# Performance work log

Measured on AMD Instinct MI355X. Metric: run time of the kernel, lower is better.

The kernel has to match this reference:

```python
import jax, jax.numpy as jnp
import numpy as np

N, D, E, TOP_K = 16384, 1024, 8, 2

def setup_inputs() -> dict:
    key = jax.random.key(0)
    ks = jax.random.split(key, 8)
    sc = 1.0 / np.sqrt(D)
    return {
        "x": jax.random.normal(ks[0], (N, D), dtype=jnp.float32),
        "context_vector": jax.random.uniform(ks[1], (E,), dtype=jnp.float32),
        "router_w": jax.random.uniform(ks[2], (E, D), minval=-sc, maxval=sc),
        "router_b": jax.random.uniform(ks[3], (E,), minval=-sc, maxval=sc),
        "expert_w": jax.random.uniform(ks[4], (E, D, D), minval=-sc, maxval=sc),
        "expert_b": jax.random.uniform(ks[5], (E, D), minval=-sc, maxval=sc),
        "context_weight": jax.random.uniform(ks[6], (1,), dtype=jnp.float32),
    }

def reference(x, context_vector, router_w, router_b, expert_w, expert_b, context_weight):
    # Router: gate logits with conceptual context bias. [N, E]
    gate_logits = x @ router_w.T + router_b + context_weight * context_vector
    weights = jax.nn.softmax(gate_logits, axis=-1)

    # Top-k selection and renormalization. [N, k]
    top_k_weights, top_k_indices = jax.lax.top_k(weights, TOP_K)
    top_k_weights = top_k_weights / jnp.sum(top_k_weights, axis=-1, keepdims=True)

    # All-expert outputs (dense grouped GEMM): y[n,e,:] = x[n] @ W[e].T + b[e]
    all_out = jnp.einsum('nd,efd->nef', x, expert_w) + expert_b  # [N, E, D]

    # Gather the top-k expert outputs per token and combine. [N, k, D]
    gathered = jnp.take_along_axis(all_out, top_k_indices[:, :, None], axis=1)
    expert_outputs = jnp.sum(top_k_weights[:, :, None] * gathered, axis=1)  # [N, D]

    # Load-balancing loss: avg router prob . fraction of tokens routed per expert
    avg_router_prob = weights.mean(axis=0)  # [E]
    assignment_mask = jax.nn.one_hot(top_k_indices, E).sum(axis=1)  # [N, E]
    fraction_routed = assignment_mask.mean(axis=0)  # [E]
    load_loss = jnp.sum(avg_router_prob * fraction_routed)

    return expert_outputs, load_loss
```

## Files before the change

### kernel.cpp

```cpp
#include <hip/hip_runtime.h>
#include <stdint.h>

#define N_TOK 16384
#define DDIM  1024
#define NEXP  8
#define CNT_STRIDE 64

#define BM 128
#define BN 128
#define BK 64
#define MAX_TILES 264
#define EP_PITCH 72

typedef __bf16 bf16x8 __attribute__((ext_vector_type(8)));
typedef float  f32x4  __attribute__((ext_vector_type(4)));

__device__ __forceinline__ unsigned short f2bf(float f) {
  union { float f; uint32_t u; } a; a.f = f;
  uint32_t u = a.u;
  u += 0x7fffu + ((u >> 16) & 1u);
  return (unsigned short)(u >> 16);
}

__device__ __forceinline__ float bf2f(unsigned short u) {
  union { uint32_t u; float f; } a; a.u = ((uint32_t)u) << 16;
  return a.f;
}

__device__ __forceinline__ float2 bfpair(uint32_t u) {
  union { uint32_t u; float f; } lo, hi;
  lo.u = u << 16; hi.u = u & 0xffff0000u;
  return make_float2(lo.f, hi.f);
}

__device__ __forceinline__ void load_lds16(const void* g, void* l) {
  __builtin_amdgcn_global_load_lds(
      (const __attribute__((address_space(1))) void*)g,
      (__attribute__((address_space(3))) void*)l,
      16, 0, 0);
}

__global__ __launch_bounds__(512) void router_kernel(
    const float* __restrict__ x, const float* __restrict__ rw,
    const float* __restrict__ rb, const float* __restrict__ cv,
    const float* __restrict__ cwp,
    const float4* __restrict__ ew4, ushort4* __restrict__ wb4,
    unsigned short* __restrict__ xg,
    int* __restrict__ perm_idx, float* __restrict__ perm_w,
    int* __restrict__ inv_idx,
    int* __restrict__ cnt, float* __restrict__ sum_w)
{
  __shared__ int   sCnt[NEXP];
  __shared__ int   sBase[NEXP];
  __shared__ float sSW[NEXP];
  __shared__ int   sE0[32], sE1[32], sR0[32], sR1[32];
  __shared__ float sW0[32], sW1[32];

  const int tid = threadIdx.x;
  if (tid < NEXP) { sCnt[tid] = 0; sSW[tid] = 0.0f; }
  __syncthreads();

  const int wave = tid >> 6;
  const int lane = tid & 63;

  float lsw[NEXP];
#pragma unroll
  for (int e = 0; e < NEXP; ++e) lsw[e] = 0.0f;

  const float cw = cwp[0];

  for (int t = 0; t < 4; ++t) {
    const int i = wave * 4 + t;
    const int n = blockIdx.x * 32 + i;

    float p[NEXP];
#pragma unroll
    for (int e = 0; e < NEXP; ++e) p[e] = 0.0f;

    const float2* x2 = (const float2*)(x + (size_t)n * DDIM);
    uint32_t* xgp = (uint32_t*)(xg + (size_t)n * DDIM);

    float2 xv[8];
#pragma unroll
    for (int it = 0; it < 8; ++it) xv[it] = x2[lane + 64 * it];
#pragma unroll
    for (int it = 0; it < 8; ++it) {
      int dp = lane + 64 * it;
      xgp[dp] = (uint32_t)f2bf(xv[it].x) | ((uint32_t)f2bf(xv[it].y) << 16);
#pragma unroll
      for (int e = 0; e < NEXP; ++e) {
        float2 wv = ((const float2*)(rw + e * DDIM))[dp];
        p[e] = fmaf(xv[it].x, wv.x, fmaf(xv[it].y, wv.y, p[e]));
      }
    }
#pragma unroll
    for (int e = 0; e < NEXP; ++e) {
#pragma unroll
      for (int off = 32; off > 0; off >>= 1)
        p[e] += __shfl_xor(p[e], off, 64);
    }

    if (lane == 0) {
      float w[NEXP];
      float m = -1e30f;
#pragma unroll
      for (int e = 0; e < NEXP; ++e) {
        w[e] = p[e] + rb[e] + cw * cv[e];
        m = fmaxf(m, w[e]);
      }
      float s = 0.0f;
#pragma unroll
      for (int e = 0; e < NEXP; ++e) { w[e] = expf(w[e] - m); s += w[e]; }
      float inv = 1.0f / s;
#pragma unroll
      for (int e = 0; e < NEXP; ++e) { w[e] *= inv; lsw[e] += w[e]; }
      int e0 = 0;
#pragma unroll
      for (int e = 1; e < NEXP; ++e) if (w[e] > w[e0]) e0 = e;
      int e1 = (e0 == 0) ? 1 : 0;
#pragma unroll
      for (int e = 0; e < NEXP; ++e) if (e != e0 && w[e] > w[e1]) e1 = e;
      float rsum = 1.0f / (w[e0] + w[e1]);
      int r0 = atomicAdd(&sCnt[e0], 1);
      int r1 = atomicAdd(&sCnt[e1], 1);
      sE0[i] = e0; sE1[i] = e1; sR0[i] = r0; sR1[i] = r1;
      sW0[i] = w[e0] * rsum; sW1[i] = w[e1] * rsum;
    }
  }

  if (lane == 0) {
#pragma unroll
    for (int e = 0; e < NEXP; ++e) atomicAdd(&sSW[e], lsw[e]);
  }
  __syncthreads();

  if (tid < NEXP) {
    sBase[tid] = atomicAdd(&cnt[tid * CNT_STRIDE], sCnt[tid]);
    atomicAdd(&sum_w[tid * CNT_STRIDE], sSW[tid]);
  }
  __syncthreads();

  if (tid < 64) {
    int i = tid >> 1, k = tid & 1;
    int e = k ? sE1[i] : sE0[i];
    int r = k ? sR1[i] : sR0[i];
    float wv = k ? sW1[i] : sW0[i];
    int pos = sBase[e] + r;
    int n = blockIdx.x * 32 + i;
    perm_idx[e * N_TOK + pos] = n;
    perm_w [e * N_TOK + pos] = wv;
    inv_idx[2 * n + k] = (e << 14) | pos;
  }

  size_t base = (size_t)blockIdx.x * 512 + tid;
#pragma unroll
  for (int i2 = 0; i2 < 8; ++i2) {
    size_t idx = base + (size_t)i2 * 262144;
    float4 v = ew4[idx];
    wb4[idx] = make_ushort4(f2bf(v.x), f2bf(v.y), f2bf(v.z), f2bf(v.w));
  }
}

template<int MODE>
__global__ __launch_bounds__(256) void moe_gemm_kernel(
    const unsigned short* __restrict__ xg, const unsigned short* __restrict__ wb,
    const float* __restrict__ eb,
    const int* __restrict__ perm_idx, const float* __restrict__ perm_w,
    const int* __restrict__ cnt,
    unsigned short* __restrict__ ybuf, float* __restrict__ out)
{
  const int id = blockIdx.x;
  const int tn = id / MAX_TILES;
  const int tileIdx = id - tn * MAX_TILES;

  int e = -1, tm = 0, count = 0, ebase = 0, pref = 0;
#pragma unroll
  for (int j = 0; j < NEXP; ++j) {
    int c = cnt[j * CNT_STRIDE];
    int t = (c + BM - 1) >> 7;
    if (e < 0 && tileIdx < pref + t) { e = j; tm = tileIdx - pref; count = c; }
    if (e < 0) ebase += c;
    pref += t;
  }
  if (e < 0) return;

  __shared__ union {
    struct { __bf16 As[BM * BK]; __bf16 Bs[BN * BK]; } g;
    __bf16 ep[4 * 64 * EP_PITCH];
  } sm;
  __shared__ int   tokS[BM];
  __shared__ float wtS[BM];

  const int tid = threadIdx.x;
  const int wave = tid >> 6;
  const int lane = tid & 63;

  if (tid < BM) {
    int row = tm * BM + tid;
    int rc = row < count ? row : count - 1;
    tokS[tid] = perm_idx[e * N_TOK + rc];
    wtS[tid] = (row < count) ? perm_w[e * N_TOK + row] : 0.0f;
  }
  __syncthreads();

  const unsigned short* aptr[4];
  const unsigned short* bptr[4];
  const unsigned short* wbase = wb + (size_t)e * DDIM * DDIM;
#pragma unroll
  for (int t = 0; t < 4; ++t) {
    int r = wave * 32 + t * 8 + (lane >> 3);
    int cg = (lane & 7) ^ (r & 7);
    aptr[t] = xg + (size_t)tokS[r] * DDIM + cg * 8;
    bptr[t] = wbase + (size_t)(tn * BN + r) * DDIM + cg * 8;
  }

  const int mw = (wave >> 1) * 64;
  const int nw = (wave & 1) * 64;
  const int quad = lane >> 4;
  const int l15 = lane & 15;

  f32x4 acc[4][4] = {};

  for (int kk = 0; kk < DDIM; kk += BK) {
#pragma unroll
    for (int t = 0; t < 4; ++t) {
      load_lds16(aptr[t], &sm.g.As[(wave * 32 + t * 8) * BK]);
      load_lds16(bptr[t], &sm.g.Bs[(wave * 32 + t * 8) * BK]);
      aptr[t] += BK; bptr[t] += BK;
    }
    __syncthreads();

#pragma unroll
    for (int ks = 0; ks < 2; ++ks) {
      bf16x8 af[4], bfr[4];
#pragma unroll
      for (int mi = 0; mi < 4; ++mi) {
        int m = mw + mi * 16 + l15;
        int slot = (ks * 4 + quad) ^ (m & 7);
        af[mi] = *(const bf16x8*)&sm.g.As[m * BK + slot * 8];
      }
#pragma unroll
      for (int ni = 0; ni < 4; ++ni) {
        int n = nw + ni * 16 + l15;
        int slot = (ks * 4 + quad) ^ (n & 7);
        bfr[ni] = *(const bf16x8*)&sm.g.Bs[n * BK + slot * 8];
      }
#pragma unroll
      for (int mi = 0; mi < 4; ++mi)
#pragma unroll
        for (int ni = 0; ni < 4; ++ni)
          acc[mi][ni] = __builtin_amdgcn_mfma_f32_16x16x32_bf16(bfr[ni], af[mi], acc[mi][ni], 0, 0, 0);
    }
    __syncthreads();
  }

  const int valid = count - tm * BM;

  if (MODE == 1) {
    __bf16* slab = &sm.ep[wave * (64 * EP_PITCH)];
#pragma unroll
    for (int mi = 0; mi < 4; ++mi) {
      float wt = wtS[mw + mi * 16 + l15];
#pragma unroll
      for (int ni = 0; ni < 4; ++ni) {
        int gcol = tn * BN + nw + ni * 16 + quad * 4;
        const float4 bv = *(const float4*)&eb[e * DDIM + gcol];
        ushort4 pk;
        pk.x = f2bf((acc[mi][ni][0] + bv.x) * wt);
        pk.y = f2bf((acc[mi][ni][1] + bv.y) * wt);
        pk.z = f2bf((acc[mi][ni][2] + bv.z) * wt);
        pk.w = f2bf((acc[mi][ni][3] + bv.w) * wt);
        *(ushort4*)&slab[(mi * 16 + l15) * EP_PITCH + ni * 16 + quad * 4] = pk;
      }
    }
    const int gb = ebase + tm * BM;
#pragma unroll
    for (int s = 0; s < 8; ++s) {
      int lrow = s * 8 + (lane >> 3);
      uint4 v = *(const uint4*)&slab[lrow * EP_PITCH + (lane & 7) * 8];
      int brow = mw + lrow;
      if (brow < valid)
        *(uint4*)&ybuf[(size_t)(gb + brow) * DDIM + tn * BN + nw + (lane & 7) * 8] = v;
    }
  } else {
#pragma unroll
    for (int mi = 0; mi < 4; ++mi) {
      int brow = mw + mi * 16 + l15;
      float wt = wtS[brow];
      int tok = tokS[brow];
#pragma unroll
      for (int ni = 0; ni < 4; ++ni) {
        int gcol = tn * BN + nw + ni * 16 + quad * 4;
        const float4 bv = *(const float4*)&eb[e * DDIM + gcol];
        if (brow < valid) {
          atomicAdd(out + (size_t)tok * DDIM + gcol + 0, (acc[mi][ni][0] + bv.x) * wt);
          atomicAdd(out + (size_t)tok * DDIM + gcol + 1, (acc[mi][ni][1] + bv.y) * wt);
          atomicAdd(out + (size_t)tok * DDIM + gcol + 2, (acc[mi][ni][2] + bv.z) * wt);
          atomicAdd(out + (size_t)tok * DDIM + gcol + 3, (acc[mi][ni][3] + bv.w) * wt);
        }
      }
    }
  }
}

__global__ __launch_bounds__(256) void combine_kernel(
    const unsigned short* __restrict__ ybuf, const int* __restrict__ inv_idx,
    const int* __restrict__ cnt, float* __restrict__ out)
{
  const int wave = threadIdx.x >> 6;
  const int lane = threadIdx.x & 63;
  const int n = blockIdx.x * 4 + wave;

  int base[NEXP];
  int acc = 0;
#pragma unroll
  for (int j = 0; j < NEXP; ++j) { base[j] = acc; acc += cnt[j * CNT_STRIDE]; }

  int i0 = inv_idx[2 * n];
  int i1 = inv_idx[2 * n + 1];
  int g0 = base[i0 >> 14] + (i0 & 16383);
  int g1 = base[i1 >> 14] + (i1 & 16383);

  const uint4* r0 = (const uint4*)(ybuf + (size_t)g0 * DDIM);
  const uint4* r1 = (const uint4*)(ybuf + (size_t)g1 * DDIM);
  float4* o = (float4*)(out + (size_t)n * DDIM);

#pragma unroll
  for (int it = 0; it < 2; ++it) {
    int c = lane + 64 * it;
    uint4 a = r0[c];
    uint4 b = r1[c];
    float2 a0 = bfpair(a.x), a1 = bfpair(a.y), a2 = bfpair(a.z), a3 = bfpair(a.w);
    float2 b0 = bfpair(b.x), b1 = bfpair(b.y), b2 = bfpair(b.z), b3 = bfpair(b.w);
    float4 v0, v1;
    v0.x = a0.x + b0.x; v0.y = a0.y + b0.y; v0.z = a1.x + b1.x; v0.w = a1.y + b1.y;
    v1.x = a2.x + b2.x; v1.y = a2.y + b2.y; v1.z = a3.x + b3.x; v1.w = a3.y + b3.y;
    o[2 * c] = v0;
    o[2 * c + 1] = v1;
  }
}

__global__ void loss_kernel(const float* __restrict__ sum_w,
                            const int* __restrict__ cnt,
                            float* __restrict__ out) {
  if (threadIdx.x == 0 && blockIdx.x == 0) {
    float l = 0.0f;
#pragma unroll
    for (int e = 0; e < NEXP; ++e)
      l += sum_w[e * CNT_STRIDE] * (float)cnt[e * CNT_STRIDE];
    out[(size_t)N_TOK * DDIM] = l * (1.0f / ((float)N_TOK * (float)N_TOK));
  }
}

extern "C" void kernel_launch(void* const* d_in, const int* in_sizes, int n_in,
                              void* d_out, int out_size, void* d_ws, size_t ws_size,
                              hipStream_t stream) {
  const float* x  = (const float*)d_in[0];
  const float* cv = (const float*)d_in[1];
  const float* rw = (const float*)d_in[2];
  const float* rb = (const float*)d_in[3];
  const float* ew = (const float*)d_in[4];
  const float* eb = (const float*)d_in[5];
  const float* cw = (const float*)d_in[6];
  float* out = (float*)d_out;

  char* ws = (char*)d_ws;
  unsigned short* xg = (unsigned short*)ws;
  unsigned short* wb = (unsigned short*)(ws + 33554432);
  int*   perm_idx = (int*)  (ws + 50331648);
  float* perm_w   = (float*)(ws + 50855936);
  int*   inv_idx  = (int*)  (ws + 51380224);
  int*   cnt      = (int*)  (ws + 51511296);
  float* sum_w    = (float*)(ws + 51513344);
  unsigned short* ybuf = (unsigned short*)(ws + 51515392);
  const size_t NEED = 51515392ull + 67108864ull;

  const bool big = ws_size >= NEED;

  hipMemsetAsync(cnt, 0, 4096, stream);
  if (!big)
    hipMemsetAsync(d_out, 0, (size_t)N_TOK * DDIM * sizeof(float), stream);

  router_kernel<<<N_TOK / 32, 512, 0, stream>>>(x, rw, rb, cv, cw,
                                                (const float4*)ew, (ushort4*)wb,
                                                xg, perm_idx, perm_w, inv_idx, cnt, sum_w);

  if (big) {
    moe_gemm_kernel<1><<<MAX_TILES * 8, 256, 0, stream>>>(
        xg, wb, eb, perm_idx, perm_w, cnt, ybuf, out);
    combine_kernel<<<N_TOK / 4, 256, 0, stream>>>(ybuf, inv_idx, cnt, out);
  } else {
    moe_gemm_kernel<0><<<MAX_TILES * 8, 256, 0, stream>>>(
        xg, wb, eb, perm_idx, perm_w, cnt, ybuf, out);
  }

  loss_kernel<<<1, 64, 0, stream>>>(sum_w, cnt, out);
}
```

Before: 288.7 us.

## Use 256x256 tiles with double-buffered LDS and interleaved MFMA/load pipeline

Enlarges the grouped-GEMM tile from 128x128 to 256x256 with 512 threads and double-buffers the A/B LDS tiles. The K loop is split into four phases, each issuing a slice of the next tile's global-to-LDS loads between MFMA groups, with hand-placed s_waitcnt barriers and raised wave priority around the MFMA blocks. This is meant to raise arithmetic intensity and hide global load latency behind compute. In exchange it uses more LDS and registers per block, pads partially filled expert tiles more heavily at the larger tile size, and produces fewer blocks, which can hurt load balance across CUs.

```diff
diff --git a/kernel.cpp b/kernel.cpp
--- a/kernel.cpp
+++ b/kernel.cpp
@@ -6,10 +6,11 @@
 #define NEXP  8
 #define CNT_STRIDE 64
 
-#define BM 128
-#define BN 128
+#define BM 256
+#define BN 256
 #define BK 64
-#define MAX_TILES 264
+#define NKT 16
+#define MAX_TILES 136
 #define EP_PITCH 72
 
 typedef __bf16 bf16x8 __attribute__((ext_vector_type(8)));
@@ -39,6 +40,11 @@
       (__attribute__((address_space(3))) void*)l,
       16, 0, 0);
 }
+
+#define SCHED_FENCE() __builtin_amdgcn_sched_barrier(0)
+#define BAR_PLAIN() do { SCHED_FENCE(); asm volatile("s_barrier" ::: "memory"); SCHED_FENCE(); } while (0)
+#define BAR_LGKM0() do { SCHED_FENCE(); asm volatile("s_waitcnt lgkmcnt(0)\n\ts_barrier" ::: "memory"); SCHED_FENCE(); } while (0)
+#define BAR_VM(N)   do { SCHED_FENCE(); asm volatile("s_waitcnt vmcnt(" #N ")\n\ts_barrier" ::: "memory"); SCHED_FENCE(); } while (0)
 
 __global__ __launch_bounds__(512) void router_kernel(
     const float* __restrict__ x, const float* __restrict__ rw,
@@ -162,7 +168,7 @@
 }
 
 template<int MODE>
-__global__ __launch_bounds__(256) void moe_gemm_kernel(
+__global__ __launch_bounds__(512, 2) void moe_gemm_kernel(
     const unsigned short* __restrict__ xg, const unsigned short* __restrict__ wb,
     const float* __restrict__ eb,
     const int* __restrict__ perm_idx, const float* __restrict__ perm_w,
@@ -177,7 +183,7 @@
 #pragma unroll
   for (int j = 0; j < NEXP; ++j) {
     int c = cnt[j * CNT_STRIDE];
-    int t = (c + BM - 1) >> 7;
+    int t = (c + BM - 1) >> 8;
     if (e < 0 && tileIdx < pref + t) { e = j; tm = tileIdx - pref; count = c; }
     if (e < 0) ebase += c;
     pref += t;
@@ -185,8 +191,8 @@
   if (e < 0) return;
 
   __shared__ union {
-    struct { __bf16 As[BM * BK]; __bf16 Bs[BN * BK]; } g;
-    __bf16 ep[4 * 64 * EP_PITCH];
+    struct { __bf16 As[2][BM * BK]; __bf16 Bs[2][BN * BK]; } g;
+    __bf16 ep[8 * 64 * EP_PITCH];
   } sm;
   __shared__ int   tokS[BM];
   __shared__ float wtS[BM];
@@ -203,96 +209,167 @@
   }
   __syncthreads();
 
-  const unsigned short* aptr[4];
-  const unsigned short* bptr[4];
   const unsigned short* wbase = wb + (size_t)e * DDIM * DDIM;
-#pragma unroll
-  for (int t = 0; t < 4; ++t) {
-    int r = wave * 32 + t * 8 + (lane >> 3);
-    int cg = (lane & 7) ^ (r & 7);
-    aptr[t] = xg + (size_t)tokS[r] * DDIM + cg * 8;
-    bptr[t] = wbase + (size_t)(tn * BN + r) * DDIM + cg * 8;
-  }
-
-  const int mw = (wave >> 1) * 64;
-  const int nw = (wave & 1) * 64;
+  const int rl = wave * 16 + (lane >> 3);
+  const int cg = (((lane & 7) ^ (lane >> 3)) & 7) * 8;
+
+  const unsigned short* gA[2][2];
+  const unsigned short* gB[2][2];
+#pragma unroll
+  for (int h = 0; h < 2; ++h)
+#pragma unroll
+    for (int j = 0; j < 2; ++j) {
+      gA[h][j] = xg + (size_t)tokS[h * 128 + rl + j * 8] * DDIM + cg;
+      gB[h][j] = wbase + (size_t)(tn * BN + h * 128 + rl + j * 8) * DDIM + cg;
+    }
+
+#define STG_A(h, bsel) do { \
+    load_lds16(gA[h][0], &sm.g.As[bsel][((h) * 128 + wave * 16) * BK]);     gA[h][0] += BK; \
+    load_lds16(gA[h][1], &sm.g.As[bsel][((h) * 128 + wave * 16 + 8) * BK]); gA[h][1] += BK; \
+  } while (0)
+#define STG_B(h, bsel) do { \
+    load_lds16(gB[h][0], &sm.g.Bs[bsel][((h) * 128 + wave * 16) * BK]);     gB[h][0] += BK; \
+    load_lds16(gB[h][1], &sm.g.Bs[bsel][((h) * 128 + wave * 16 + 8) * BK]); gB[h][1] += BK; \
+  } while (0)
+
+  STG_A(0, 0); STG_A(1, 0); STG_B(0, 0); STG_B(1, 0);
+  STG_A(0, 1);
+  BAR_VM(0);
+
+  const int wr = wave >> 2;
+  const int wc = wave & 3;
   const int quad = lane >> 4;
   const int l15 = lane & 15;
-
-  f32x4 acc[4][4] = {};
-
-  for (int kk = 0; kk < DDIM; kk += BK) {
-#pragma unroll
-    for (int t = 0; t < 4; ++t) {
-      load_lds16(aptr[t], &sm.g.As[(wave * 32 + t * 8) * BK]);
-      load_lds16(bptr[t], &sm.g.Bs[(wave * 32 + t * 8) * BK]);
-      aptr[t] += BK; bptr[t] += BK;
-    }
-    __syncthreads();
-
-#pragma unroll
-    for (int ks = 0; ks < 2; ++ks) {
-      bf16x8 af[4], bfr[4];
-#pragma unroll
-      for (int mi = 0; mi < 4; ++mi) {
-        int m = mw + mi * 16 + l15;
-        int slot = (ks * 4 + quad) ^ (m & 7);
-        af[mi] = *(const bf16x8*)&sm.g.As[m * BK + slot * 8];
-      }
-#pragma unroll
-      for (int ni = 0; ni < 4; ++ni) {
-        int n = nw + ni * 16 + l15;
-        int slot = (ks * 4 + quad) ^ (n & 7);
-        bfr[ni] = *(const bf16x8*)&sm.g.Bs[n * BK + slot * 8];
-      }
+  const int sl0 = (quad ^ (l15 & 7)) * 8;
+  const int rowA = (wr * 128 + l15) * BK + sl0;
+  const int rowB = (wc * 64 + l15) * BK + sl0;
+
+  f32x4 acc[8][4] = {};
+
+#pragma unroll
+  for (int t = 0; t < NKT; ++t) {
+    const int b = t & 1, nb = b ^ 1;
+    const __bf16* Ab = sm.g.As[b];
+    const __bf16* Bb = sm.g.Bs[b];
+    bf16x8 Bf[4][2], Af[4][2];
+
+    if (t + 1 < NKT) STG_A(1, nb);
+#pragma unroll
+    for (int ni = 0; ni < 2; ++ni)
+#pragma unroll
+      for (int ks = 0; ks < 2; ++ks)
+        Bf[ni][ks] = *(const bf16x8*)&Bb[(rowB + ni * 1024) ^ (ks * 32)];
+#pragma unroll
+    for (int mi = 0; mi < 4; ++mi)
+#pragma unroll
+      for (int ks = 0; ks < 2; ++ks)
+        Af[mi][ks] = *(const bf16x8*)&Ab[(rowA + mi * 1024) ^ (ks * 32)];
+    __builtin_amdgcn_s_setprio(1);
+#pragma unroll
+    for (int ks = 0; ks < 2; ++ks)
 #pragma unroll
       for (int mi = 0; mi < 4; ++mi)
 #pragma unroll
-        for (int ni = 0; ni < 4; ++ni)
-          acc[mi][ni] = __builtin_amdgcn_mfma_f32_16x16x32_bf16(bfr[ni], af[mi], acc[mi][ni], 0, 0, 0);
-    }
-    __syncthreads();
-  }
+        for (int ni = 0; ni < 2; ++ni)
+          acc[mi][ni] = __builtin_amdgcn_mfma_f32_16x16x32_bf16(Bf[ni][ks], Af[mi][ks], acc[mi][ni], 0, 0, 0);
+    __builtin_amdgcn_s_setprio(0);
+    BAR_PLAIN();
+
+    if (t + 1 < NKT) STG_B(0, nb);
+#pragma unroll
+    for (int ni = 2; ni < 4; ++ni)
+#pragma unroll
+      for (int ks = 0; ks < 2; ++ks)
+        Bf[ni][ks] = *(const bf16x8*)&Bb[(rowB + ni * 1024) ^ (ks * 32)];
+    __builtin_amdgcn_s_setprio(1);
+#pragma unroll
+    for (int ks = 0; ks < 2; ++ks)
+#pragma unroll
+      for (int mi = 0; mi < 4; ++mi)
+#pragma unroll
+        for (int ni = 2; ni < 4; ++ni)
+          acc[mi][ni] = __builtin_amdgcn_mfma_f32_16x16x32_bf16(Bf[ni][ks], Af[mi][ks], acc[mi][ni], 0, 0, 0);
+    __builtin_amdgcn_s_setprio(0);
+    BAR_PLAIN();
+
+    if (t + 1 < NKT) STG_B(1, nb);
+#pragma unroll
+    for (int mi = 0; mi < 4; ++mi)
+#pragma unroll
+      for (int ks = 0; ks < 2; ++ks)
+        Af[mi][ks] = *(const bf16x8*)&Ab[(rowA + (mi + 4) * 1024) ^ (ks * 32)];
+    __builtin_amdgcn_s_setprio(1);
+#pragma unroll
+    for (int ks = 0; ks < 2; ++ks)
+#pragma unroll
+      for (int mi = 0; mi < 4; ++mi)
+#pragma unroll
+        for (int ni = 0; ni < 2; ++ni)
+          acc[mi + 4][ni] = __builtin_amdgcn_mfma_f32_16x16x32_bf16(Bf[ni][ks], Af[mi][ks], acc[mi + 4][ni], 0, 0, 0);
+    __builtin_amdgcn_s_setprio(0);
+    BAR_LGKM0();
+
+    if (t + 2 < NKT) STG_A(0, b);
+    __builtin_amdgcn_s_setprio(1);
+#pragma unroll
+    for (int ks = 0; ks < 2; ++ks)
+#pragma unroll
+      for (int mi = 0; mi < 4; ++mi)
+#pragma unroll
+        for (int ni = 2; ni < 4; ++ni)
+          acc[mi + 4][ni] = __builtin_amdgcn_mfma_f32_16x16x32_bf16(Bf[ni][ks], Af[mi][ks], acc[mi + 4][ni], 0, 0, 0);
+    __builtin_amdgcn_s_setprio(0);
+    if (t + 2 < NKT)      BAR_VM(2);
+    else if (t + 1 < NKT) BAR_VM(0);
+    else                  BAR_PLAIN();
+  }
+
+#undef STG_A
+#undef STG_B
 
   const int valid = count - tm * BM;
+  const int gb = ebase + tm * BM;
 
   if (MODE == 1) {
     __bf16* slab = &sm.ep[wave * (64 * EP_PITCH)];
 #pragma unroll
-    for (int mi = 0; mi < 4; ++mi) {
-      float wt = wtS[mw + mi * 16 + l15];
-#pragma unroll
-      for (int ni = 0; ni < 4; ++ni) {
-        int gcol = tn * BN + nw + ni * 16 + quad * 4;
-        const float4 bv = *(const float4*)&eb[e * DDIM + gcol];
-        ushort4 pk;
-        pk.x = f2bf((acc[mi][ni][0] + bv.x) * wt);
-        pk.y = f2bf((acc[mi][ni][1] + bv.y) * wt);
-        pk.z = f2bf((acc[mi][ni][2] + bv.z) * wt);
-        pk.w = f2bf((acc[mi][ni][3] + bv.w) * wt);
-        *(ushort4*)&slab[(mi * 16 + l15) * EP_PITCH + ni * 16 + quad * 4] = pk;
+    for (int p = 0; p < 2; ++p) {
+#pragma unroll
+      for (int mi4 = 0; mi4 < 4; ++mi4) {
+        const int mi = p * 4 + mi4;
+        float wt = wtS[wr * 128 + mi * 16 + l15];
+#pragma unroll
+        for (int ni = 0; ni < 4; ++ni) {
+          int gcol = tn * BN + wc * 64 + ni * 16 + quad * 4;
+          const float4 bv = *(const float4*)&eb[e * DDIM + gcol];
+          ushort4 pk;
+          pk.x = f2bf((acc[mi][ni][0] + bv.x) * wt);
+          pk.y = f2bf((acc[mi][ni][1] + bv.y) * wt);
+          pk.z = f2bf((acc[mi][ni][2] + bv.z) * wt);
+          pk.w = f2bf((acc[mi][ni][3] + bv.w) * wt);
+          *(ushort4*)&slab[(mi4 * 16 + l15) * EP_PITCH + ni * 16 + quad * 4] = pk;
+        }
       }
-    }
-    const int gb = ebase + tm * BM;
-#pragma unroll
-    for (int s = 0; s < 8; ++s) {
-      int lrow = s * 8 + (lane >> 3);
-      uint4 v = *(const uint4*)&slab[lrow * EP_PITCH + (lane & 7) * 8];
-      int brow = mw + lrow;
-      if (brow < valid)
-        *(uint4*)&ybuf[(size_t)(gb + brow) * DDIM + tn * BN + nw + (lane & 7) * 8] = v;
+#pragma unroll
+      for (int s = 0; s < 8; ++s) {
+        int lrow = s * 8 + (lane >> 3);
+        uint4 v = *(const uint4*)&slab[lrow * EP_PITCH + (lane & 7) * 8];
+        int brow = wr * 128 + p * 64 + lrow;
+        if (brow < valid)
+          *(uint4*)&ybuf[(size_t)(gb + brow) * DDIM + tn * BN + wc * 64 + (lane & 7) * 8] = v;
+      }
     }
   } else {
 #pragma unroll
-    for (int mi = 0; mi < 4; ++mi) {
-      int brow = mw + mi * 16 + l15;
+    for (int mi = 0; mi < 8; ++mi) {
+      int brow = wr * 128 + mi * 16 + l15;
       float wt = wtS[brow];
       int tok = tokS[brow];
-#pragma unroll
-      for (int ni = 0; ni < 4; ++ni) {
-        int gcol = tn * BN + nw + ni * 16 + quad * 4;
-        const float4 bv = *(const float4*)&eb[e * DDIM + gcol];
-        if (brow < valid) {
+      if (brow < valid) {
+#pragma unroll
+        for (int ni = 0; ni < 4; ++ni) {
+          int gcol = tn * BN + wc * 64 + ni * 16 + quad * 4;
+          const float4 bv = *(const float4*)&eb[e * DDIM + gcol];
           atomicAdd(out + (size_t)tok * DDIM + gcol + 0, (acc[mi][ni][0] + bv.x) * wt);
           atomicAdd(out + (size_t)tok * DDIM + gcol + 1, (acc[mi][ni][1] + bv.y) * wt);
           atomicAdd(out + (size_t)tok * DDIM + gcol + 2, (acc[mi][ni][2] + bv.z) * wt);
@@ -386,11 +463,11 @@
                                                 xg, perm_idx, perm_w, inv_idx, cnt, sum_w);
 
   if (big) {
-    moe_gemm_kernel<1><<<MAX_TILES * 8, 256, 0, stream>>>(
+    moe_gemm_kernel<1><<<MAX_TILES * 4, 512, 0, stream>>>(
         xg, wb, eb, perm_idx, perm_w, cnt, ybuf, out);
     combine_kernel<<<N_TOK / 4, 256, 0, stream>>>(ybuf, inv_idx, cnt, out);
   } else {
-    moe_gemm_kernel<0><<<MAX_TILES * 8, 256, 0, stream>>>(
+    moe_gemm_kernel<0><<<MAX_TILES * 4, 512, 0, stream>>>(
         xg, wb, eb, perm_idx, perm_w, cnt, ybuf, out);
   }
 
```

After: 305.9 us. 1.06x slower.

## Double-buffer LDS in MoE GEMM and batch router loads across tokens

Applied to the files above, without the earlier changes.

The GEMM main loop now uses two LDS buffers, so the global-to-LDS loads for the next K tile are issued before the MFMAs on the current tile, with one barrier per iteration using explicit waitcnt and scheduling fences. The loop is fully unrolled and launch bounds request two blocks per CU. The router kernel is restructured to handle four tokens per wave at once with float4 loads, reusing each router weight load across those tokens. The aim is to hide global load latency behind compute and cut redundant router weight traffic, at the cost of doubled LDS use and more register pressure.

```diff
diff --git a/kernel.cpp b/kernel.cpp
--- a/kernel.cpp
+++ b/kernel.cpp
@@ -9,6 +9,7 @@
 #define BM 128
 #define BN 128
 #define BK 64
+#define NKT 16
 #define MAX_TILES 264
 #define EP_PITCH 72
 
@@ -39,6 +40,10 @@
       (__attribute__((address_space(3))) void*)l,
       16, 0, 0);
 }
+
+#define SCHED_FENCE() __builtin_amdgcn_sched_barrier(0)
+#define BAR_PLAIN() do { SCHED_FENCE(); asm volatile("s_barrier" ::: "memory"); SCHED_FENCE(); } while (0)
+#define BAR_VM0()   do { SCHED_FENCE(); asm volatile("s_waitcnt vmcnt(0)\n\ts_barrier" ::: "memory"); SCHED_FENCE(); } while (0)
 
 __global__ __launch_bounds__(512) void router_kernel(
     const float* __restrict__ x, const float* __restrict__ rw,
@@ -62,50 +67,69 @@
 
   const int wave = tid >> 6;
   const int lane = tid & 63;
+  const int n0 = blockIdx.x * 32 + wave * 4;
+
+  const float cw = cwp[0];
+  const float4* rw4 = (const float4*)rw;
+
+  const float4* x4[4];
+  uint2* xgp[4];
+#pragma unroll
+  for (int t = 0; t < 4; ++t) {
+    x4[t]  = (const float4*)(x + (size_t)(n0 + t) * DDIM);
+    xgp[t] = (uint2*)(xg + (size_t)(n0 + t) * DDIM);
+  }
+
+  float p[4][NEXP];
+#pragma unroll
+  for (int t = 0; t < 4; ++t)
+#pragma unroll
+    for (int e = 0; e < NEXP; ++e) p[t][e] = 0.0f;
+
+#pragma unroll
+  for (int it = 0; it < 4; ++it) {
+    const int dp = lane + 64 * it;
+    float4 wv[NEXP];
+#pragma unroll
+    for (int e = 0; e < NEXP; ++e) wv[e] = rw4[e * 256 + dp];
+#pragma unroll
+    for (int t = 0; t < 4; ++t) {
+      float4 xv = x4[t][dp];
+      uint2 pk;
+      pk.x = (uint32_t)f2bf(xv.x) | ((uint32_t)f2bf(xv.y) << 16);
+      pk.y = (uint32_t)f2bf(xv.z) | ((uint32_t)f2bf(xv.w) << 16);
+      xgp[t][dp] = pk;
+#pragma unroll
+      for (int e = 0; e < NEXP; ++e)
+        p[t][e] = fmaf(xv.x, wv[e].x,
+                  fmaf(xv.y, wv[e].y,
+                  fmaf(xv.z, wv[e].z,
+                  fmaf(xv.w, wv[e].w, p[t][e]))));
+    }
+  }
+
+#pragma unroll
+  for (int t = 0; t < 4; ++t)
+#pragma unroll
+    for (int e = 0; e < NEXP; ++e) {
+#pragma unroll
+      for (int off = 32; off > 0; off >>= 1)
+        p[t][e] += __shfl_xor(p[t][e], off, 64);
+    }
 
   float lsw[NEXP];
 #pragma unroll
   for (int e = 0; e < NEXP; ++e) lsw[e] = 0.0f;
 
-  const float cw = cwp[0];
-
+#pragma unroll
   for (int t = 0; t < 4; ++t) {
     const int i = wave * 4 + t;
-    const int n = blockIdx.x * 32 + i;
-
-    float p[NEXP];
-#pragma unroll
-    for (int e = 0; e < NEXP; ++e) p[e] = 0.0f;
-
-    const float2* x2 = (const float2*)(x + (size_t)n * DDIM);
-    uint32_t* xgp = (uint32_t*)(xg + (size_t)n * DDIM);
-
-    float2 xv[8];
-#pragma unroll
-    for (int it = 0; it < 8; ++it) xv[it] = x2[lane + 64 * it];
-#pragma unroll
-    for (int it = 0; it < 8; ++it) {
-      int dp = lane + 64 * it;
-      xgp[dp] = (uint32_t)f2bf(xv[it].x) | ((uint32_t)f2bf(xv[it].y) << 16);
-#pragma unroll
-      for (int e = 0; e < NEXP; ++e) {
-        float2 wv = ((const float2*)(rw + e * DDIM))[dp];
-        p[e] = fmaf(xv[it].x, wv.x, fmaf(xv[it].y, wv.y, p[e]));
-      }
-    }
-#pragma unroll
-    for (int e = 0; e < NEXP; ++e) {
-#pragma unroll
-      for (int off = 32; off > 0; off >>= 1)
-        p[e] += __shfl_xor(p[e], off, 64);
-    }
-
     if (lane == 0) {
       float w[NEXP];
       float m = -1e30f;
 #pragma unroll
       for (int e = 0; e < NEXP; ++e) {
-        w[e] = p[e] + rb[e] + cw * cv[e];
+        w[e] = p[t][e] + rb[e] + cw * cv[e];
         m = fmaxf(m, w[e]);
       }
       float s = 0.0f;
@@ -162,7 +186,7 @@
 }
 
 template<int MODE>
-__global__ __launch_bounds__(256) void moe_gemm_kernel(
+__global__ __launch_bounds__(256, 2) void moe_gemm_kernel(
     const unsigned short* __restrict__ xg, const unsigned short* __restrict__ wb,
     const float* __restrict__ eb,
     const int* __restrict__ perm_idx, const float* __restrict__ perm_w,
@@ -185,7 +209,7 @@
   if (e < 0) return;
 
   __shared__ union {
-    struct { __bf16 As[BM * BK]; __bf16 Bs[BN * BK]; } g;
+    struct { __bf16 As[2][BM * BK]; __bf16 Bs[2][BN * BK]; } g;
     __bf16 ep[4 * 64 * EP_PITCH];
   } sm;
   __shared__ int   tokS[BM];
@@ -203,9 +227,9 @@
   }
   __syncthreads();
 
+  const unsigned short* wbase = wb + (size_t)e * DDIM * DDIM;
   const unsigned short* aptr[4];
   const unsigned short* bptr[4];
-  const unsigned short* wbase = wb + (size_t)e * DDIM * DDIM;
 #pragma unroll
   for (int t = 0; t < 4; ++t) {
     int r = wave * 32 + t * 8 + (lane >> 3);
@@ -214,6 +238,18 @@
     bptr[t] = wbase + (size_t)(tn * BN + r) * DDIM + cg * 8;
   }
 
+#define STG_ALL(bsel) do { \
+    _Pragma("unroll") \
+    for (int t4 = 0; t4 < 4; ++t4) { \
+      load_lds16(aptr[t4], &sm.g.As[bsel][(wave * 32 + t4 * 8) * BK]); \
+      load_lds16(bptr[t4], &sm.g.Bs[bsel][(wave * 32 + t4 * 8) * BK]); \
+      aptr[t4] += BK; bptr[t4] += BK; \
+    } \
+  } while (0)
+
+  STG_ALL(0);
+  BAR_VM0();
+
   const int mw = (wave >> 1) * 64;
   const int nw = (wave & 1) * 64;
   const int quad = lane >> 4;
@@ -221,14 +257,13 @@
 
   f32x4 acc[4][4] = {};
 
-  for (int kk = 0; kk < DDIM; kk += BK) {
-#pragma unroll
-    for (int t = 0; t < 4; ++t) {
-      load_lds16(aptr[t], &sm.g.As[(wave * 32 + t * 8) * BK]);
-      load_lds16(bptr[t], &sm.g.Bs[(wave * 32 + t * 8) * BK]);
-      aptr[t] += BK; bptr[t] += BK;
-    }
-    __syncthreads();
+#pragma unroll
+  for (int kt = 0; kt < NKT; ++kt) {
+    const int b = kt & 1, nb = b ^ 1;
+    const __bf16* Ab = sm.g.As[b];
+    const __bf16* Bb = sm.g.Bs[b];
+
+    if (kt + 1 < NKT) STG_ALL(nb);
 
 #pragma unroll
     for (int ks = 0; ks < 2; ++ks) {
@@ -237,13 +272,13 @@
       for (int mi = 0; mi < 4; ++mi) {
         int m = mw + mi * 16 + l15;
         int slot = (ks * 4 + quad) ^ (m & 7);
-        af[mi] = *(const bf16x8*)&sm.g.As[m * BK + slot * 8];
+        af[mi] = *(const bf16x8*)&Ab[m * BK + slot * 8];
       }
 #pragma unroll
       for (int ni = 0; ni < 4; ++ni) {
         int n = nw + ni * 16 + l15;
         int slot = (ks * 4 + quad) ^ (n & 7);
-        bfr[ni] = *(const bf16x8*)&sm.g.Bs[n * BK + slot * 8];
+        bfr[ni] = *(const bf16x8*)&Bb[n * BK + slot * 8];
       }
 #pragma unroll
       for (int mi = 0; mi < 4; ++mi)
@@ -251,10 +286,15 @@
         for (int ni = 0; ni < 4; ++ni)
           acc[mi][ni] = __builtin_amdgcn_mfma_f32_16x16x32_bf16(bfr[ni], af[mi], acc[mi][ni], 0, 0, 0);
     }
-    __syncthreads();
-  }
+
+    if (kt + 1 < NKT) BAR_VM0();
+    else             BAR_PLAIN();
+  }
+
+#undef STG_ALL
 
   const int valid = count - tm * BM;
+  const int gb = ebase + tm * BM;
 
   if (MODE == 1) {
     __bf16* slab = &sm.ep[wave * (64 * EP_PITCH)];
@@ -273,7 +313,6 @@
         *(ushort4*)&slab[(mi * 16 + l15) * EP_PITCH + ni * 16 + quad * 4] = pk;
       }
     }
-    const int gb = ebase + tm * BM;
 #pragma unroll
     for (int s = 0; s < 8; ++s) {
       int lrow = s * 8 + (lane >> 3);
```

After: 297.6 us. +3.1%, slower.
